# Kernel tuning notes

Measured on AMD Instinct MI355X. Metric: run time of the kernel, lower is better.

## Reference

```python
import jax, jax.numpy as jnp
import numpy as np

SAMPLE_RATE = 0.1
BINS = int(256 * SAMPLE_RATE)  # 25
KSIZE = 7
EPS = 1e-6


def _pascal_kernel_2d(ksize):
    # kornia get_pascal_kernel_2d(ksize, norm=True): outer product of binomial row, sum=1
    row = np.array([1.0, 6.0, 15.0, 20.0, 15.0, 6.0, 1.0], dtype=np.float32)
    row = row / row.sum()
    k2d = np.outer(row, row)
    return jnp.asarray(k2d, dtype=jnp.float32)


def _blur_pool2d(x, ksize=KSIZE):
    # kornia.filters.blur_pool2d: depthwise conv with pascal kernel, stride 2, zero pad ksize//2
    C = x.shape[1]
    k = jnp.broadcast_to(_pascal_kernel_2d(ksize).astype(x.dtype), (C, 1, ksize, ksize))
    pad = ksize // 2
    return jax.lax.conv_general_dilated(
        x, k, window_strides=(2, 2), padding=((pad, pad), (pad, pad)),
        feature_group_count=C, dimension_numbers=("NCHW", "OIHW", "NCHW"))


def _per_channel_hist(x, bins):
    # torch.histc(v, bins, 0, 1) per (b, c) plane: values outside [0,1] ignored,
    # value == 1 falls in last bin. Fused via one flat scatter-add.
    B, C, H, W = x.shape
    v = x.reshape(B * C, H * W)
    idx = jnp.clip(jnp.floor(v * bins).astype(jnp.int32), 0, bins - 1)
    valid = ((v >= 0.0) & (v <= 1.0)).astype(x.dtype)
    flat_idx = (jnp.arange(B * C, dtype=jnp.int32)[:, None] * bins + idx).reshape(-1)
    hist = jnp.zeros(B * C * bins, dtype=x.dtype).at[flat_idx].add(valid.reshape(-1))
    return hist.reshape(B, C, bins)


def setup_inputs() -> dict:
    key = jax.random.key(0)
    kx, ky = jax.random.split(key)
    B, C, H, W = 32, 3, 512, 512
    x = jax.random.uniform(kx, (B, C, H, W), dtype=jnp.float32)
    y = jax.random.uniform(ky, (B, C, H, W), dtype=jnp.float32)
    return {"x": x, "y": y}


def reference(x, y):
    hw = x.shape[-2] * x.shape[-1]  # original H*W (as in source)
    xb = _blur_pool2d(x)
    yb = _blur_pool2d(y)
    xh = _per_channel_hist(xb, BINS) / hw  # [B, C, BINS]
    yh = _per_channel_hist(yb, BINS) / hw
    # nn.CosineSimilarity(dim=0, eps=1e-6) applied per (b, c) vector pair
    dot = jnp.sum(xh * yh, axis=-1)
    nx = jnp.maximum(jnp.linalg.norm(xh, axis=-1), EPS)
    ny = jnp.maximum(jnp.linalg.norm(yh, axis=-1), EPS)
    cos = dot / (nx * ny)  # [B, C]
    return jnp.mean(cos)
```

## Files before the change

kernel.cpp:

```cpp
#include <hip/hip_runtime.h>

#define BINS 25
#define H 512
#define W 512
#define NPLANES 96
#define NSH 32

__global__ __launch_bounds__(256) void blur_hist(
        const float* __restrict__ x, const float* __restrict__ y,
        unsigned int* __restrict__ partial) {
    const int b = blockIdx.x;
    const int z = b >> 2;
    const float* src = (z < NPLANES) ? x + (size_t)z * H * W
                                     : y + (size_t)(z - NPLANES) * H * W;

    __shared__ unsigned int sh[NSH * BINS];
    const int tid = threadIdx.x;
    if (tid < (NSH * BINS / 4))
        *(float4*)((float*)sh + 4 * tid) = make_float4(0.f, 0.f, 0.f, 0.f);
    __syncthreads();

    const int i = tid & 63;
    const int s = (b & 3) * 4 + (tid >> 6);
    const int c0 = 8 * i - 4;
    const int o0 = (i == 0)  ? 0   : c0;
    const int o3 = (i == 63) ? 508 : c0 + 12;
    const float m0 = (i == 0)  ? 0.f : 1.f;
    const float m3 = (i == 63) ? 0.f : 1.f;

    const float w0 = 1.f/64.f, w1 = 6.f/64.f, w2 = 15.f/64.f, w3 = 20.f/64.f;

    auto load_row = [&](int gy) -> float4 {
        float4 h = make_float4(0.f, 0.f, 0.f, 0.f);
        if ((unsigned)gy < (unsigned)H) {
            const float* rp = src + (size_t)gy * W;
            float4 Q0 = *(const float4*)(rp + o0);
            float4 Q1 = *(const float4*)(rp + c0 + 4);
            float4 Q2 = *(const float4*)(rp + c0 + 8);
            float4 Q3 = *(const float4*)(rp + o3);
            float r1 = Q0.y * m0, r2 = Q0.z * m0, r3 = Q0.w * m0;
            float r4 = Q1.x, r5 = Q1.y, r6 = Q1.z, r7 = Q1.w;
            float r8 = Q2.x, r9 = Q2.y, r10 = Q2.z, r11 = Q2.w;
            float r12 = Q3.x * m3, r13 = Q3.y * m3;
            h.x = w0*(r1 + r7)  + w1*(r2 + r6)  + w2*(r3 + r5)  + w3*r4;
            h.y = w0*(r3 + r9)  + w1*(r4 + r8)  + w2*(r5 + r7)  + w3*r6;
            h.z = w0*(r5 + r11) + w1*(r6 + r10) + w2*(r7 + r9)  + w3*r8;
            h.w = w0*(r7 + r13) + w1*(r8 + r12) + w2*(r9 + r11) + w3*r10;
        }
        return h;
    };

    unsigned int* wh = sh + (tid & (NSH - 1)) * BINS;
    auto binit = [&](float v) {
        int bb = min((int)(v * 25.f), BINS - 1);
        atomicAdd(&wh[bb], 1u);
    };
    auto vout = [&](const float4& h0, const float4& h1, const float4& h2,
                    const float4& h3, const float4& h4, const float4& h5,
                    const float4& h6) {
        binit(w0*(h0.x+h6.x) + w1*(h1.x+h5.x) + w2*(h2.x+h4.x) + w3*h3.x);
        binit(w0*(h0.y+h6.y) + w1*(h1.y+h5.y) + w2*(h2.y+h4.y) + w3*h3.y);
        binit(w0*(h0.z+h6.z) + w1*(h1.z+h5.z) + w2*(h2.z+h4.z) + w3*h3.z);
        binit(w0*(h0.w+h6.w) + w1*(h1.w+h5.w) + w2*(h2.w+h4.w) + w3*h3.w);
    };

    const int gy0 = 32 * s - 3;
    float4 h0 = load_row(gy0 + 0), h1 = load_row(gy0 + 1), h2 = load_row(gy0 + 2),
           h3 = load_row(gy0 + 3), h4 = load_row(gy0 + 4), h5 = load_row(gy0 + 5),
           h6 = load_row(gy0 + 6);
    #pragma unroll 5
    for (int j = 0; j < 15; j++) {
        float4 hA = load_row(gy0 + 7 + 2 * j);
        float4 hB = load_row(gy0 + 8 + 2 * j);
        vout(h0, h1, h2, h3, h4, h5, h6);
        h0 = h2; h1 = h3; h2 = h4; h3 = h5; h4 = h6; h5 = hA; h6 = hB;
    }
    vout(h0, h1, h2, h3, h4, h5, h6);
    __syncthreads();

    if (tid < BINS) {
        unsigned int acc = 0;
        #pragma unroll
        for (int g = 0; g < NSH; g++) acc += sh[g * BINS + tid];
        partial[b * BINS + tid] = acc;
    }
}

__global__ __launch_bounds__(64) void reduce_cos(
        const unsigned int* __restrict__ partial, float* __restrict__ out) {
    __shared__ float sa[BINS], sb[BINS];
    const int p = blockIdx.x;
    const int t = threadIdx.x;
    if (t < BINS) {
        unsigned int a = 0, bb = 0;
        #pragma unroll
        for (int j = 0; j < 4; j++) {
            a  += partial[((size_t)p * 4 + j) * BINS + t];
            bb += partial[((size_t)(NPLANES + p) * 4 + j) * BINS + t];
        }
        sa[t] = (float)a;
        sb[t] = (float)bb;
    }
    __syncthreads();
    if (t == 0) {
        const float inv_hw = 1.0f / (float)(H * W);
        float dot = 0.f, nx = 0.f, ny = 0.f;
        for (int k = 0; k < BINS; k++) {
            float a = sa[k] * inv_hw;
            float c = sb[k] * inv_hw;
            dot += a * c;
            nx  += a * a;
            ny  += c * c;
        }
        nx = fmaxf(sqrtf(nx), 1e-6f);
        ny = fmaxf(sqrtf(ny), 1e-6f);
        atomicAdd(out, (dot / (nx * ny)) * (1.0f / (float)NPLANES));
    }
}

extern "C" void kernel_launch(void* const* d_in, const int* in_sizes, int n_in,
                              void* d_out, int out_size, void* d_ws, size_t ws_size,
                              hipStream_t stream) {
    const float* x = (const float*)d_in[0];
    const float* y = (const float*)d_in[1];
    float* out = (float*)d_out;

    unsigned int* partial = (unsigned int*)d_ws;

    hipMemsetAsync(out, 0, sizeof(float), stream);

    blur_hist<<<768, 256, 0, stream>>>(x, y, partial);
    reduce_cos<<<NPLANES, 64, 0, stream>>>(partial, out);
}
```

Baseline: 221.4 us.

## Software-pipeline raw row loads three steps ahead and remap blocks across XCDs

Raw row loads are split from the horizontal blur. Three pairs of raw rows are kept in flight in registers, so global loads are issued several output rows ahead of their use. Block indices are permuted so consecutive launched blocks map to different plane groups, and launch bounds request at least three blocks per CU. The deeper prefetch raises register pressure and may cut occupancy or cause spills.

```diff
diff --git a/kernel.cpp b/kernel.cpp
--- a/kernel.cpp
+++ b/kernel.cpp
@@ -5,11 +5,12 @@
 #define W 512
 #define NPLANES 96
 #define NSH 32
+#define BPP 4
 
-__global__ __launch_bounds__(256) void blur_hist(
+__global__ __launch_bounds__(256, 3) void blur_hist(
         const float* __restrict__ x, const float* __restrict__ y,
         unsigned int* __restrict__ partial) {
-    const int b = blockIdx.x;
+    const int b = ((blockIdx.x & 7) * 96) + (blockIdx.x >> 3);
     const int z = b >> 2;
     const float* src = (z < NPLANES) ? x + (size_t)z * H * W
                                      : y + (size_t)(z - NPLANES) * H * W;
@@ -30,23 +31,28 @@
 
     const float w0 = 1.f/64.f, w1 = 6.f/64.f, w2 = 15.f/64.f, w3 = 20.f/64.f;
 
-    auto load_row = [&](int gy) -> float4 {
-        float4 h = make_float4(0.f, 0.f, 0.f, 0.f);
+    auto RAW = [&](int gy, float4& qa, float4& qb, float4& qc, float4& qd) {
         if ((unsigned)gy < (unsigned)H) {
             const float* rp = src + (size_t)gy * W;
-            float4 Q0 = *(const float4*)(rp + o0);
-            float4 Q1 = *(const float4*)(rp + c0 + 4);
-            float4 Q2 = *(const float4*)(rp + c0 + 8);
-            float4 Q3 = *(const float4*)(rp + o3);
-            float r1 = Q0.y * m0, r2 = Q0.z * m0, r3 = Q0.w * m0;
-            float r4 = Q1.x, r5 = Q1.y, r6 = Q1.z, r7 = Q1.w;
-            float r8 = Q2.x, r9 = Q2.y, r10 = Q2.z, r11 = Q2.w;
-            float r12 = Q3.x * m3, r13 = Q3.y * m3;
-            h.x = w0*(r1 + r7)  + w1*(r2 + r6)  + w2*(r3 + r5)  + w3*r4;
-            h.y = w0*(r3 + r9)  + w1*(r4 + r8)  + w2*(r5 + r7)  + w3*r6;
-            h.z = w0*(r5 + r11) + w1*(r6 + r10) + w2*(r7 + r9)  + w3*r8;
-            h.w = w0*(r7 + r13) + w1*(r8 + r12) + w2*(r9 + r11) + w3*r10;
+            qa = *(const float4*)(rp + o0);
+            qb = *(const float4*)(rp + c0 + 4);
+            qc = *(const float4*)(rp + c0 + 8);
+            qd = *(const float4*)(rp + o3);
+        } else {
+            qa = qb = qc = qd = make_float4(0.f, 0.f, 0.f, 0.f);
         }
+    };
+    auto HB = [&](const float4& qa, const float4& qb,
+                  const float4& qc, const float4& qd) -> float4 {
+        float r1 = qa.y * m0, r2 = qa.z * m0, r3 = qa.w * m0;
+        float r4 = qb.x, r5 = qb.y, r6 = qb.z, r7 = qb.w;
+        float r8 = qc.x, r9 = qc.y, r10 = qc.z, r11 = qc.w;
+        float r12 = qd.x * m3, r13 = qd.y * m3;
+        float4 h;
+        h.x = w0*(r1 + r7)  + w1*(r2 + r6)  + w2*(r3 + r5)  + w3*r4;
+        h.y = w0*(r3 + r9)  + w1*(r4 + r8)  + w2*(r5 + r7)  + w3*r6;
+        h.z = w0*(r5 + r11) + w1*(r6 + r10) + w2*(r7 + r9)  + w3*r8;
+        h.w = w0*(r7 + r13) + w1*(r8 + r12) + w2*(r9 + r11) + w3*r10;
         return h;
     };
 
@@ -65,17 +71,53 @@
     };
 
     const int gy0 = 32 * s - 3;
-    float4 h0 = load_row(gy0 + 0), h1 = load_row(gy0 + 1), h2 = load_row(gy0 + 2),
-           h3 = load_row(gy0 + 3), h4 = load_row(gy0 + 4), h5 = load_row(gy0 + 5),
-           h6 = load_row(gy0 + 6);
-    #pragma unroll 5
-    for (int j = 0; j < 15; j++) {
-        float4 hA = load_row(gy0 + 7 + 2 * j);
-        float4 hB = load_row(gy0 + 8 + 2 * j);
-        vout(h0, h1, h2, h3, h4, h5, h6);
-        h0 = h2; h1 = h3; h2 = h4; h3 = h5; h4 = h6; h5 = hA; h6 = hB;
+
+    float4 A0,A1,A2,A3,A4,A5,A6,A7;
+    float4 B0,B1,B2,B3,B4,B5,B6,B7;
+    float4 C0,C1,C2,C3,C4,C5,C6,C7;
+    RAW(gy0 + 7,  A0,A1,A2,A3);  RAW(gy0 + 8,  A4,A5,A6,A7);
+    RAW(gy0 + 9,  B0,B1,B2,B3);  RAW(gy0 + 10, B4,B5,B6,B7);
+    RAW(gy0 + 11, C0,C1,C2,C3);  RAW(gy0 + 12, C4,C5,C6,C7);
+
+    float4 h0, h1, h2, h3, h4, h5, h6;
+    {
+        float4 qa, qb, qc, qd;
+        RAW(gy0 + 0, qa,qb,qc,qd); h0 = HB(qa,qb,qc,qd);
+        RAW(gy0 + 1, qa,qb,qc,qd); h1 = HB(qa,qb,qc,qd);
+        RAW(gy0 + 2, qa,qb,qc,qd); h2 = HB(qa,qb,qc,qd);
+        RAW(gy0 + 3, qa,qb,qc,qd); h3 = HB(qa,qb,qc,qd);
+        RAW(gy0 + 4, qa,qb,qc,qd); h4 = HB(qa,qb,qc,qd);
+        RAW(gy0 + 5, qa,qb,qc,qd); h5 = HB(qa,qb,qc,qd);
+        RAW(gy0 + 6, qa,qb,qc,qd); h6 = HB(qa,qb,qc,qd);
     }
-    vout(h0, h1, h2, h3, h4, h5, h6);
+
+    float4 hA, hB;
+    #pragma unroll 1
+    for (int j = 0; j < 4; j++) {
+        const int r = gy0 + 6 * j;
+        hA = HB(A0,A1,A2,A3); hB = HB(A4,A5,A6,A7);
+        RAW(r + 13, A0,A1,A2,A3); RAW(r + 14, A4,A5,A6,A7);
+        vout(h0,h1,h2,h3,h4,h5,h6);
+        h0=h2; h1=h3; h2=h4; h3=h5; h4=h6; h5=hA; h6=hB;
+        hA = HB(B0,B1,B2,B3); hB = HB(B4,B5,B6,B7);
+        RAW(r + 15, B0,B1,B2,B3); RAW(r + 16, B4,B5,B6,B7);
+        vout(h0,h1,h2,h3,h4,h5,h6);
+        h0=h2; h1=h3; h2=h4; h3=h5; h4=h6; h5=hA; h6=hB;
+        hA = HB(C0,C1,C2,C3); hB = HB(C4,C5,C6,C7);
+        RAW(r + 17, C0,C1,C2,C3); RAW(r + 18, C4,C5,C6,C7);
+        vout(h0,h1,h2,h3,h4,h5,h6);
+        h0=h2; h1=h3; h2=h4; h3=h5; h4=h6; h5=hA; h6=hB;
+    }
+    hA = HB(A0,A1,A2,A3); hB = HB(A4,A5,A6,A7);
+    vout(h0,h1,h2,h3,h4,h5,h6);
+    h0=h2; h1=h3; h2=h4; h3=h5; h4=h6; h5=hA; h6=hB;
+    hA = HB(B0,B1,B2,B3); hB = HB(B4,B5,B6,B7);
+    vout(h0,h1,h2,h3,h4,h5,h6);
+    h0=h2; h1=h3; h2=h4; h3=h5; h4=h6; h5=hA; h6=hB;
+    hA = HB(C0,C1,C2,C3); hB = HB(C4,C5,C6,C7);
+    vout(h0,h1,h2,h3,h4,h5,h6);
+    h0=h2; h1=h3; h2=h4; h3=h5; h4=h6; h5=hA; h6=hB;
+    vout(h0,h1,h2,h3,h4,h5,h6);
     __syncthreads();
 
     if (tid < BINS) {
@@ -94,9 +136,9 @@
     if (t < BINS) {
         unsigned int a = 0, bb = 0;
         #pragma unroll
-        for (int j = 0; j < 4; j++) {
-            a  += partial[((size_t)p * 4 + j) * BINS + t];
-            bb += partial[((size_t)(NPLANES + p) * 4 + j) * BINS + t];
+        for (int j = 0; j < BPP; j++) {
+            a  += partial[((size_t)p * BPP + j) * BINS + t];
+            bb += partial[((size_t)(NPLANES + p) * BPP + j) * BINS + t];
         }
         sa[t] = (float)a;
         sb[t] = (float)bb;
@@ -129,6 +171,6 @@
 
     hipMemsetAsync(out, 0, sizeof(float), stream);
 
-    blur_hist<<<768, 256, 0, stream>>>(x, y, partial);
+    blur_hist<<<2 * NPLANES * BPP, 256, 0, stream>>>(x, y, partial);
     reduce_cos<<<NPLANES, 64, 0, stream>>>(partial, out);
 }
```

New measurement: 275.1 us. 24.3% more time.
